# Optimization experiments

Measured on AMD Instinct MI355X. Metric: run time of the kernel, lower is better.

The kernel has to match this reference:

```python
import jax, jax.numpy as jnp
import numpy as np

N = 100000   # nodes
E = 1600000  # edges
IN = 128     # in_dim
H = 128      # hidden
C = 9        # num_classes
G = 256      # graphs in batch


def setup_inputs() -> dict:
    key = jax.random.key(0)
    ks = jax.random.split(key, 24)
    w = lambda k, shp: jax.random.normal(k, shp, dtype=jnp.float32) * 0.05
    inp = {
        "x": jax.random.normal(ks[0], (N, IN), dtype=jnp.float32),
        "edge_index": jax.random.randint(ks[1], (2, E), 0, N, dtype=jnp.int32),
        "batch": jnp.sort(jax.random.randint(ks[2], (N,), 0, G, dtype=jnp.int32)),
        # GIN layer 0 MLP: Linear(IN,H) -> ReLU -> Linear(H,H)
        "l0_w1": w(ks[3], (IN, H)), "l0_b1": jnp.zeros((H,), jnp.float32),
        "l0_w2": w(ks[4], (H, H)),  "l0_b2": jnp.zeros((H,), jnp.float32),
        # GIN layer 1 MLP
        "l1_w1": w(ks[5], (H, H)), "l1_b1": jnp.zeros((H,), jnp.float32),
        "l1_w2": w(ks[6], (H, H)), "l1_b2": jnp.zeros((H,), jnp.float32),
        # GlobalAttention gate: Linear(H,1)
        "gate_w": w(ks[7], (H, 1)), "gate_b": jnp.zeros((1,), jnp.float32),
        # classification head: Linear(H,H) -> ReLU -> Linear(H,C)
        "cls_w1": w(ks[8], (H, H)), "cls_b1": jnp.zeros((H,), jnp.float32),
        "cls_w2": w(ks[9], (H, C)), "cls_b2": jnp.zeros((C,), jnp.float32),
        "reg_w1": w(ks[10], (H, H)), "reg_b1": jnp.zeros((H,), jnp.float32),
        "reg_w2": w(ks[11], (H, 1)), "reg_b2": jnp.zeros((1,), jnp.float32),
    }
    return inp


def reference(x, edge_index, batch,
              l0_w1, l0_b1, l0_w2, l0_b2,
              l1_w1, l1_b1, l1_w2, l1_b2,
              gate_w, gate_b,
              cls_w1, cls_b1, cls_w2, cls_b2,
              reg_w1, reg_b1, reg_w2, reg_b2):
    src, dst = edge_index[0], edge_index[1]

    def gin_layer(h, w1, b1, w2, b2):
        # GINConv with eps=0: (1+eps)*h + sum_{j in N(i)} h_j, then MLP, then outer ReLU
        agg = jax.ops.segment_sum(h[src], dst, num_segments=N)
        z = h + agg
        z = jax.nn.relu(z @ w1 + b1) @ w2 + b2
        return jax.nn.relu(z)

    h = gin_layer(x, l0_w1, l0_b1, l0_w2, l0_b2)
    h = gin_layer(h, l1_w1, l1_b1, l1_w2, l1_b2)

    # GlobalAttention readout: per-graph segment softmax over gate scores
    gate = (h @ gate_w + gate_b)[:, 0]                      # [N]
    m = jax.ops.segment_max(gate, batch, num_segments=G)    # [G]
    a = jnp.exp(gate - m[batch])                            # [N]
    denom = jax.ops.segment_sum(a, batch, num_segments=G)   # [G]
    wgt = a / denom[batch]                                  # [N]
    g = jax.ops.segment_sum(h * wgt[:, None], batch, num_segments=G)  # [G, H]

    cls = jax.nn.relu(g @ cls_w1 + cls_b1) @ cls_w2 + cls_b2
    reg = jax.nn.relu(g @ reg_w1 + reg_b1) @ reg_w2 + reg_b2
    return cls, reg
```

## Files before the change

kernel.cpp:

```cpp
#include <hip/hip_runtime.h>
#include <hip/hip_fp16.h>

#define N_NODES 100000
#define N_EDGES 1600000
#define HDIM    128
#define NGRAPH  256
#define NRES    8
#define PAD     64

typedef __attribute__((ext_vector_type(8))) short short8;
typedef __attribute__((ext_vector_type(8))) _Float16 half8;
typedef __attribute__((ext_vector_type(4))) float f32x4;

__device__ inline uint pkadd(uint a, uint b) {
    __half2 r = __hadd2(__builtin_bit_cast(__half2, a), __builtin_bit_cast(__half2, b));
    return __builtin_bit_cast(uint, r);
}
__device__ inline ushort f2h(float x) { return __half_as_ushort(__float2half_rn(x)); }
__device__ inline float h2f(ushort h) { return __half2float(__ushort_as_half(h)); }

__global__ __launch_bounds__(256) void scatter_pad_kernel(
        const int* __restrict__ src, const int* __restrict__ dst,
        int* __restrict__ cnt, int* __restrict__ eadj, int E) {
    int res  = blockIdx.x & (NRES - 1);
    int grp  = blockIdx.x >> 3;
    int ngrp = gridDim.x >> 3;
    int lo = res * (N_NODES / NRES), hi = lo + (N_NODES / NRES);
    for (int e = grp * 256 + threadIdx.x; e < E; e += ngrp * 256) {
        int d = dst[e];
        if (d >= lo && d < hi) {
            int p = atomicAdd(&cnt[d], 1);
            if (p < PAD) eadj[d * PAD + p] = src[e];
        }
    }
}

__global__ __launch_bounds__(256) void f2h_kernel(const float* __restrict__ x,
                                                  ushort* __restrict__ xh, int n4) {
    for (int i = blockIdx.x * 256 + threadIdx.x; i < n4; i += gridDim.x * 256) {
        float4 v = ((const float4*)x)[i];
        ushort4 o;
        o.x = f2h(v.x); o.y = f2h(v.y); o.z = f2h(v.z); o.w = f2h(v.w);
        ((ushort4*)xh)[i] = o;
    }
}

__global__ void pack4_kernel(const float* __restrict__ wa, const float* __restrict__ wb,
                             const float* __restrict__ wc, const float* __restrict__ wd,
                             ushort* __restrict__ ha, ushort* __restrict__ la,
                             ushort* __restrict__ hb, ushort* __restrict__ lb,
                             ushort* __restrict__ hc, ushort* __restrict__ lc,
                             ushort* __restrict__ hd, ushort* __restrict__ ld) {
    int sel = blockIdx.x >> 6;
    const float* w = sel == 0 ? wa : sel == 1 ? wb : sel == 2 ? wc : wd;
    ushort* hi = sel == 0 ? ha : sel == 1 ? hb : sel == 2 ? hc : hd;
    ushort* lo = sel == 0 ? la : sel == 1 ? lb : sel == 2 ? lc : ld;
    int t = (blockIdx.x & 63) * 256 + threadIdx.x;
    int i = t & 7, lane = (t >> 3) & 63, cfg = (t >> 9) & 7, ks = t >> 12;
    int k = ks * 32 + (lane >> 4) * 8 + i;
    int c = cfg * 16 + (lane & 15);
    float v = w[k * 128 + c];
    ushort h = f2h(v);
    hi[t] = h;
    lo[t] = f2h(v - h2f(h));
}

template<bool LAST>
__global__ __launch_bounds__(256, 8) void gin_layer_kernel(
        const ushort* __restrict__ hin,
        const int* __restrict__ cnt, const int* __restrict__ eadj,
        const ushort* __restrict__ w1h, const ushort* __restrict__ w1l,
        const float* __restrict__ b1,
        const ushort* __restrict__ w2h, const ushort* __restrict__ w2l,
        const float* __restrict__ b2,
        ushort* __restrict__ hout,
        const float* __restrict__ gw, const float* __restrict__ gb,
        float* __restrict__ gateb) {
    __shared__ ushort zt[32 * 128];
    __shared__ ushort tt[32 * 128];
    int tid  = threadIdx.x;
    int lane = tid & 63;
    int wv   = tid >> 6;
    int row0 = blockIdx.x * 32;
    int cfg0 = wv * 2;
    int g    = lane >> 4;
    int q    = lane & 15;
    const uint4* h4 = (const uint4*)hin;

    for (int j = 0; j < 8; j++) {
        int lr  = wv * 8 + j;
        int row = row0 + lr;
        int deg = cnt[row]; deg = deg > PAD ? PAD : deg;
        int al  = (lane < deg) ? eadj[row * PAD + lane] : 0;
        uint4 acc = make_uint4(0u, 0u, 0u, 0u);
        int nch = (deg + 4) >> 2;
        for (int c = 0; c < nch; c++) {
            int jj = 4 * c + g - 1;
            int nb = __shfl(al, jj < 0 ? 0 : jj);
            int idx = jj < 0 ? row : nb;
            if (jj < deg) {
                uint4 u = h4[idx * 16 + q];
                acc.x = pkadd(acc.x, u.x); acc.y = pkadd(acc.y, u.y);
                acc.z = pkadd(acc.z, u.z); acc.w = pkadd(acc.w, u.w);
            }
        }
        #pragma unroll
        for (int off = 16; off <= 32; off <<= 1) {
            acc.x = pkadd(acc.x, (uint)__shfl_xor((int)acc.x, off));
            acc.y = pkadd(acc.y, (uint)__shfl_xor((int)acc.y, off));
            acc.z = pkadd(acc.z, (uint)__shfl_xor((int)acc.z, off));
            acc.w = pkadd(acc.w, (uint)__shfl_xor((int)acc.w, off));
        }
        if (g == 0) {
            int boff = (lr * 256 + q * 16) ^ ((lr & 7) << 4);
            *(uint4*)((char*)zt + boff) = acc;
        }
    }
    __syncthreads();

    f32x4 acc[2][2];
    #pragma unroll
    for (int rf = 0; rf < 2; rf++)
        #pragma unroll
        for (int cf = 0; cf < 2; cf++) acc[rf][cf] = (f32x4){0.f, 0.f, 0.f, 0.f};

    for (int ks = 0; ks < 4; ks++) {
        half8 bh[2], bl[2];
        #pragma unroll
        for (int cf = 0; cf < 2; cf++) {
            int bidx = (((ks * 8 + cfg0 + cf) * 64 + lane) * 8);
            bh[cf] = __builtin_bit_cast(half8, *(const short8*)&w1h[bidx]);
            bl[cf] = __builtin_bit_cast(half8, *(const short8*)&w1l[bidx]);
        }
        #pragma unroll
        for (int rf = 0; rf < 2; rf++) {
            int r = rf * 16 + q;
            int off = (r * 256 + ks * 64 + g * 16) ^ ((r & 7) << 4);
            half8 a = __builtin_bit_cast(half8, *(const short8*)((const char*)zt + off));
            #pragma unroll
            for (int cf = 0; cf < 2; cf++) {
                acc[rf][cf] = __builtin_amdgcn_mfma_f32_16x16x32_f16(a, bh[cf], acc[rf][cf], 0, 0, 0);
                acc[rf][cf] = __builtin_amdgcn_mfma_f32_16x16x32_f16(a, bl[cf], acc[rf][cf], 0, 0, 0);
            }
        }
    }

    #pragma unroll
    for (int cf = 0; cf < 2; cf++) {
        int c = (cfg0 + cf) * 16 + q;
        float bias = b1[c];
        #pragma unroll
        for (int rf = 0; rf < 2; rf++) {
            #pragma unroll
            for (int i = 0; i < 4; i++) {
                int r = rf * 16 + g * 4 + i;
                float v = fmaxf(acc[rf][cf][i] + bias, 0.f);
                int off = (r * 256 + c * 2) ^ ((r & 7) << 4);
                *(ushort*)((char*)tt + off) = f2h(v);
            }
        }
    }
    __syncthreads();

    #pragma unroll
    for (int rf = 0; rf < 2; rf++)
        #pragma unroll
        for (int cf = 0; cf < 2; cf++) acc[rf][cf] = (f32x4){0.f, 0.f, 0.f, 0.f};

    for (int ks = 0; ks < 4; ks++) {
        half8 bh[2], bl[2];
        #pragma unroll
        for (int cf = 0; cf < 2; cf++) {
            int bidx = (((ks * 8 + cfg0 + cf) * 64 + lane) * 8);
            bh[cf] = __builtin_bit_cast(half8, *(const short8*)&w2h[bidx]);
            bl[cf] = __builtin_bit_cast(half8, *(const short8*)&w2l[bidx]);
        }
        #pragma unroll
        for (int rf = 0; rf < 2; rf++) {
            int r = rf * 16 + q;
            int off = (r * 256 + ks * 64 + g * 16) ^ ((r & 7) << 4);
            half8 a = __builtin_bit_cast(half8, *(const short8*)((const char*)tt + off));
            #pragma unroll
            for (int cf = 0; cf < 2; cf++) {
                acc[rf][cf] = __builtin_amdgcn_mfma_f32_16x16x32_f16(a, bh[cf], acc[rf][cf], 0, 0, 0);
                acc[rf][cf] = __builtin_amdgcn_mfma_f32_16x16x32_f16(a, bl[cf], acc[rf][cf], 0, 0, 0);
            }
        }
    }

    float pg[8];
    if (LAST) {
        #pragma unroll
        for (int p = 0; p < 8; p++) pg[p] = 0.f;
    }
    #pragma unroll
    for (int cf = 0; cf < 2; cf++) {
        int c = (cfg0 + cf) * 16 + q;
        float bias = b2[c];
        float gwc = LAST ? gw[c] : 0.f;
        #pragma unroll
        for (int rf = 0; rf < 2; rf++) {
            #pragma unroll
            for (int i = 0; i < 4; i++) {
                int row = row0 + rf * 16 + g * 4 + i;
                float v = fmaxf(acc[rf][cf][i] + bias, 0.f);
                if (row < N_NODES) hout[(size_t)row * 128 + c] = f2h(v);
                if (LAST) pg[rf * 4 + i] += v * gwc;
            }
        }
    }
    if (LAST) {
        #pragma unroll
        for (int off = 1; off < 16; off <<= 1)
            #pragma unroll
            for (int p = 0; p < 8; p++) pg[p] += __shfl_xor(pg[p], off);
        __syncthreads();
        float* gpart = (float*)zt;
        if (q == 0) {
            #pragma unroll
            for (int rf = 0; rf < 2; rf++)
                #pragma unroll
                for (int i = 0; i < 4; i++)
                    gpart[wv * 32 + rf * 16 + g * 4 + i] = pg[rf * 4 + i];
        }
        __syncthreads();
        if (tid < 32) {
            int row = row0 + tid;
            if (row < N_NODES)
                gateb[row] = gpart[tid] + gpart[32 + tid] + gpart[64 + tid] + gpart[96 + tid] + gb[0];
        }
    }
}

__device__ inline int lower_bound_i(const int* a, int n, int v) {
    int lo = 0, hi = n;
    while (lo < hi) {
        int mid = (lo + hi) >> 1;
        if (a[mid] < v) lo = mid + 1; else hi = mid;
    }
    return lo;
}

__global__ __launch_bounds__(512) void readout_kernel(
        const ushort* __restrict__ h2h, const float* __restrict__ gate,
        const int* __restrict__ batch,
        const float* __restrict__ cw1, const float* __restrict__ cb1,
        const float* __restrict__ cw2, const float* __restrict__ cb2,
        const float* __restrict__ rw1, const float* __restrict__ rb1,
        const float* __restrict__ rw2, const float* __restrict__ rb2,
        float* __restrict__ out) {
    int g = blockIdx.x, t = threadIdx.x;
    int wv = t >> 6, lane = t & 63;
    __shared__ int   bounds[2];
    __shared__ float red[512];
    __shared__ float part[8][128];
    __shared__ float gv[128];
    __shared__ float t1c[128], t1r[128];
    if (t == 0) {
        bounds[0] = lower_bound_i(batch, N_NODES, g);
        bounds[1] = lower_bound_i(batch, N_NODES, g + 1);
    }
    __syncthreads();
    int s = bounds[0], e = bounds[1];

    float m = -3.4e38f;
    for (int i = s + t; i < e; i += 512) m = fmaxf(m, gate[i]);
    red[t] = m;
    __syncthreads();
    for (int off = 256; off; off >>= 1) {
        if (t < off) red[t] = fmaxf(red[t], red[t + off]);
        __syncthreads();
    }
    m = red[0];
    __syncthreads();

    float dsum = 0.f;
    for (int i = s + t; i < e; i += 512) dsum += expf(gate[i] - m);
    red[t] = dsum;
    __syncthreads();
    for (int off = 256; off; off >>= 1) {
        if (t < off) red[t] += red[t + off];
        __syncthreads();
    }
    float denom = red[0];
    float invd = (e > s && denom > 0.f) ? 1.f / denom : 0.f;

    const uint* h2u = (const uint*)h2h;
    float a0 = 0.f, a1 = 0.f, b0 = 0.f, b1v = 0.f;
    int i0 = s + wv;
    for (; i0 + 8 < e; i0 += 16) {
        float w0 = expf(gate[i0] - m);
        float w1 = expf(gate[i0 + 8] - m);
        __half2 v0 = __builtin_bit_cast(__half2, h2u[(size_t)i0 * 64 + lane]);
        __half2 v1 = __builtin_bit_cast(__half2, h2u[(size_t)(i0 + 8) * 64 + lane]);
        a0 += w0 * __low2float(v0); a1 += w0 * __high2float(v0);
        b0 += w1 * __low2float(v1); b1v += w1 * __high2float(v1);
    }
    if (i0 < e) {
        float w0 = expf(gate[i0] - m);
        __half2 v0 = __builtin_bit_cast(__half2, h2u[(size_t)i0 * 64 + lane]);
        a0 += w0 * __low2float(v0); a1 += w0 * __high2float(v0);
    }
    part[wv][lane * 2]     = a0 + b0;
    part[wv][lane * 2 + 1] = a1 + b1v;
    __syncthreads();
    if (t < 128) {
        float acc = 0.f;
        #pragma unroll
        for (int w = 0; w < 8; w++) acc += part[w][t];
        gv[t] = acc * invd;
    }
    __syncthreads();

    if (t < 128) {
        float a = cb1[t];
        for (int k = 0; k < HDIM; k++) a += gv[k] * cw1[k * HDIM + t];
        t1c[t] = fmaxf(a, 0.f);
    } else if (t < 256) {
        int tf = t - 128;
        float a = rb1[tf];
        for (int k = 0; k < HDIM; k++) a += gv[k] * rw1[k * HDIM + tf];
        t1r[tf] = fmaxf(a, 0.f);
    }
    __syncthreads();

    if (t < 9) {
        float acc2 = cb2[t];
        for (int k = 0; k < HDIM; k++) acc2 += t1c[k] * cw2[k * 9 + t];
        out[g * 9 + t] = acc2;
    }
    if (t == 64) {
        float acc2 = rb2[0];
        for (int k = 0; k < HDIM; k++) acc2 += t1r[k] * rw2[k];
        out[NGRAPH * 9 + g] = acc2;
    }
}

extern "C" void kernel_launch(void* const* d_in, const int* in_sizes, int n_in,
                              void* d_out, int out_size, void* d_ws, size_t ws_size,
                              hipStream_t stream) {
    const float* x     = (const float*)d_in[0];
    const int*   ei    = (const int*)d_in[1];
    const int*   batch = (const int*)d_in[2];
    const float *l0w1 = (const float*)d_in[3],  *l0b1 = (const float*)d_in[4];
    const float *l0w2 = (const float*)d_in[5],  *l0b2 = (const float*)d_in[6];
    const float *l1w1 = (const float*)d_in[7],  *l1b1 = (const float*)d_in[8];
    const float *l1w2 = (const float*)d_in[9],  *l1b2 = (const float*)d_in[10];
    const float *gw   = (const float*)d_in[11], *gb   = (const float*)d_in[12];
    const float *cw1  = (const float*)d_in[13], *cb1  = (const float*)d_in[14];
    const float *cw2  = (const float*)d_in[15], *cb2  = (const float*)d_in[16];
    const float *rw1  = (const float*)d_in[17], *rb1  = (const float*)d_in[18];
    const float *rw2  = (const float*)d_in[19], *rb2  = (const float*)d_in[20];
    const int* src = ei;
    const int* dst = ei + N_EDGES;
    float* out = (float*)d_out;

    char* ws = (char*)d_ws;
    size_t o = 0;
    auto alloc = [&](size_t bytes) { void* p = ws + o; o = (o + bytes + 255) & ~(size_t)255; return p; };
    ushort* h2h   = (ushort*)alloc((size_t)N_NODES * HDIM * 2);
    ushort* xh    = h2h;
    ushort* h1h   = (ushort*)alloc((size_t)N_NODES * HDIM * 2);
    int*    eadj  = (int*)alloc((size_t)N_NODES * PAD * 4);
    int*    cnt   = (int*)alloc(N_NODES * 4);
    float*  gateb = (float*)alloc(N_NODES * 4);
    ushort* w0h1 = (ushort*)alloc(16384 * 2), *w0l1 = (ushort*)alloc(16384 * 2);
    ushort* w0h2 = (ushort*)alloc(16384 * 2), *w0l2 = (ushort*)alloc(16384 * 2);
    ushort* w1h1 = (ushort*)alloc(16384 * 2), *w1l1 = (ushort*)alloc(16384 * 2);
    ushort* w1h2 = (ushort*)alloc(16384 * 2), *w1l2 = (ushort*)alloc(16384 * 2);
    (void)ws_size; (void)in_sizes; (void)n_in; (void)out_size;

    pack4_kernel<<<256, 256, 0, stream>>>(l0w1, l0w2, l1w1, l1w2,
                                          w0h1, w0l1, w0h2, w0l2,
                                          w1h1, w1l1, w1h2, w1l2);

    hipMemsetAsync(cnt, 0, N_NODES * 4, stream);
    scatter_pad_kernel<<<2048, 256, 0, stream>>>(src, dst, cnt, eadj, N_EDGES);
    f2h_kernel<<<1024, 256, 0, stream>>>(x, xh, N_NODES * HDIM / 4);

    const int layerBlocks = (N_NODES + 31) / 32;
    gin_layer_kernel<false><<<layerBlocks, 256, 0, stream>>>(
        xh, cnt, eadj, w0h1, w0l1, l0b1, w0h2, w0l2, l0b2,
        h1h, gw, gb, nullptr);
    gin_layer_kernel<true><<<layerBlocks, 256, 0, stream>>>(
        h1h, cnt, eadj, w1h1, w1l1, l1b1, w1h2, w1l2, l1b2,
        h2h, gw, gb, gateb);

    readout_kernel<<<NGRAPH, 512, 0, stream>>>(h2h, gateb, batch,
                                               cw1, cb1, cw2, cb2,
                                               rw1, rb1, rw2, rb2, out);
}
```

Baseline: 282.1 us.

## Batch neighbor gathers two rows at a time and stage output stores through LDS

The aggregation loop now preloads adjacency lists and degrees for all 8 rows up front, then gathers two rows per iteration so twice as many independent global loads are in flight. The layer output is written into swizzled shared memory first and then copied out with coalesced 16-byte stores instead of scattered 2-byte stores. Bounds checks are removed because N is divisible by 32, and the wave index is made scalar with readfirstlane. This raises register pressure, which matters under the launch bound of 8, and adds an extra barrier.

```diff
diff --git a/kernel.cpp b/kernel.cpp
--- a/kernel.cpp
+++ b/kernel.cpp
@@ -15,6 +15,11 @@
 __device__ inline uint pkadd(uint a, uint b) {
     __half2 r = __hadd2(__builtin_bit_cast(__half2, a), __builtin_bit_cast(__half2, b));
     return __builtin_bit_cast(uint, r);
+}
+__device__ inline uint4 pkadd4(uint4 a, uint4 b) {
+    a.x = pkadd(a.x, b.x); a.y = pkadd(a.y, b.y);
+    a.z = pkadd(a.z, b.z); a.w = pkadd(a.w, b.w);
+    return a;
 }
 __device__ inline ushort f2h(float x) { return __half_as_ushort(__float2half_rn(x)); }
 __device__ inline float h2f(ushort h) { return __half2float(__ushort_as_half(h)); }
@@ -81,39 +86,55 @@
     int tid  = threadIdx.x;
     int lane = tid & 63;
     int wv   = tid >> 6;
+    int wvs  = __builtin_amdgcn_readfirstlane(wv);
     int row0 = blockIdx.x * 32;
-    int cfg0 = wv * 2;
+    int cfg0 = wvs * 2;
     int g    = lane >> 4;
     int q    = lane & 15;
     const uint4* h4 = (const uint4*)hin;
 
+    int baseRow = row0 + wvs * 8;
+    int al[8], dg[8];
+    #pragma unroll
     for (int j = 0; j < 8; j++) {
-        int lr  = wv * 8 + j;
-        int row = row0 + lr;
-        int deg = cnt[row]; deg = deg > PAD ? PAD : deg;
-        int al  = (lane < deg) ? eadj[row * PAD + lane] : 0;
-        uint4 acc = make_uint4(0u, 0u, 0u, 0u);
-        int nch = (deg + 4) >> 2;
+        al[j] = eadj[(baseRow + j) * PAD + lane];
+        int d = cnt[baseRow + j];
+        dg[j] = d > PAD ? PAD : d;
+    }
+
+    #pragma unroll
+    for (int jp = 0; jp < 4; jp++) {
+        int lrA = wvs * 8 + 2 * jp, lrB = lrA + 1;
+        int rowA = row0 + lrA, rowB = rowA + 1;
+        int dA = dg[2 * jp], dB = dg[2 * jp + 1];
+        uint4 accA = make_uint4(0u, 0u, 0u, 0u);
+        uint4 accB = make_uint4(0u, 0u, 0u, 0u);
+        int dmax = dA > dB ? dA : dB;
+        int nch = (dmax + 4) >> 2;
         for (int c = 0; c < nch; c++) {
             int jj = 4 * c + g - 1;
-            int nb = __shfl(al, jj < 0 ? 0 : jj);
-            int idx = jj < 0 ? row : nb;
-            if (jj < deg) {
-                uint4 u = h4[idx * 16 + q];
-                acc.x = pkadd(acc.x, u.x); acc.y = pkadd(acc.y, u.y);
-                acc.z = pkadd(acc.z, u.z); acc.w = pkadd(acc.w, u.w);
-            }
+            int s = jj < 0 ? 0 : jj;
+            int nbA = __shfl(al[2 * jp], s);
+            int nbB = __shfl(al[2 * jp + 1], s);
+            int idxA = jj < 0 ? rowA : nbA;
+            int idxB = jj < 0 ? rowB : nbB;
+            if (jj < dA) accA = pkadd4(accA, h4[idxA * 16 + q]);
+            if (jj < dB) accB = pkadd4(accB, h4[idxB * 16 + q]);
         }
         #pragma unroll
         for (int off = 16; off <= 32; off <<= 1) {
-            acc.x = pkadd(acc.x, (uint)__shfl_xor((int)acc.x, off));
-            acc.y = pkadd(acc.y, (uint)__shfl_xor((int)acc.y, off));
-            acc.z = pkadd(acc.z, (uint)__shfl_xor((int)acc.z, off));
-            acc.w = pkadd(acc.w, (uint)__shfl_xor((int)acc.w, off));
+            accA.x = pkadd(accA.x, (uint)__shfl_xor((int)accA.x, off));
+            accA.y = pkadd(accA.y, (uint)__shfl_xor((int)accA.y, off));
+            accA.z = pkadd(accA.z, (uint)__shfl_xor((int)accA.z, off));
+            accA.w = pkadd(accA.w, (uint)__shfl_xor((int)accA.w, off));
+            accB.x = pkadd(accB.x, (uint)__shfl_xor((int)accB.x, off));
+            accB.y = pkadd(accB.y, (uint)__shfl_xor((int)accB.y, off));
+            accB.z = pkadd(accB.z, (uint)__shfl_xor((int)accB.z, off));
+            accB.w = pkadd(accB.w, (uint)__shfl_xor((int)accB.w, off));
         }
         if (g == 0) {
-            int boff = (lr * 256 + q * 16) ^ ((lr & 7) << 4);
-            *(uint4*)((char*)zt + boff) = acc;
+            *(uint4*)((char*)zt + ((lrA * 256 + q * 16) ^ ((lrA & 7) << 4))) = accA;
+            *(uint4*)((char*)zt + ((lrB * 256 + q * 16) ^ ((lrB & 7) << 4))) = accB;
         }
     }
     __syncthreads();
@@ -202,32 +223,41 @@
         for (int rf = 0; rf < 2; rf++) {
             #pragma unroll
             for (int i = 0; i < 4; i++) {
-                int row = row0 + rf * 16 + g * 4 + i;
+                int r = rf * 16 + g * 4 + i;
                 float v = fmaxf(acc[rf][cf][i] + bias, 0.f);
-                if (row < N_NODES) hout[(size_t)row * 128 + c] = f2h(v);
+                int off = (r * 256 + c * 2) ^ ((r & 7) << 4);
+                *(ushort*)((char*)zt + off) = f2h(v);
                 if (LAST) pg[rf * 4 + i] += v * gwc;
             }
         }
     }
+    __syncthreads();
+
+    #pragma unroll
+    for (int p = 0; p < 2; p++) {
+        int idx = tid + 256 * p;
+        int r = idx >> 4, ch = idx & 15;
+        uint4 v = *(const uint4*)((const char*)zt + ((r * 256 + ch * 16) ^ ((r & 7) << 4)));
+        ((uint4*)hout)[(size_t)(row0 + r) * 16 + ch] = v;
+    }
+
     if (LAST) {
         #pragma unroll
         for (int off = 1; off < 16; off <<= 1)
             #pragma unroll
             for (int p = 0; p < 8; p++) pg[p] += __shfl_xor(pg[p], off);
-        __syncthreads();
-        float* gpart = (float*)zt;
+        float* gpart = (float*)tt;
         if (q == 0) {
             #pragma unroll
             for (int rf = 0; rf < 2; rf++)
                 #pragma unroll
                 for (int i = 0; i < 4; i++)
-                    gpart[wv * 32 + rf * 16 + g * 4 + i] = pg[rf * 4 + i];
+                    gpart[wvs * 32 + rf * 16 + g * 4 + i] = pg[rf * 4 + i];
         }
         __syncthreads();
         if (tid < 32) {
-            int row = row0 + tid;
-            if (row < N_NODES)
-                gateb[row] = gpart[tid] + gpart[32 + tid] + gpart[64 + tid] + gpart[96 + tid] + gb[0];
+            gateb[row0 + tid] = gpart[tid] + gpart[32 + tid] + gpart[64 + tid]
+                              + gpart[96 + tid] + gb[0];
         }
     }
 }
@@ -378,7 +408,7 @@
     scatter_pad_kernel<<<2048, 256, 0, stream>>>(src, dst, cnt, eadj, N_EDGES);
     f2h_kernel<<<1024, 256, 0, stream>>>(x, xh, N_NODES * HDIM / 4);
 
-    const int layerBlocks = (N_NODES + 31) / 32;
+    const int layerBlocks = N_NODES / 32;
     gin_layer_kernel<false><<<layerBlocks, 256, 0, stream>>>(
         xh, cnt, eadj, w0h1, w0l1, l0b1, w0h2, w0l2, l0b2,
         h1h, gw, gb, nullptr);
```

Result: slower. 288.7 us (+2.3%).
